# Kernel optimization log

Hardware: AMD Instinct MI355X
Metric: run time of the kernel (lower is better)

## Reference

```python
import jax, jax.numpy as jnp
import numpy as np

B, V, S = 128, 64, 40
D, H, VOC = 256, 256, 20000


def setup_inputs() -> dict:
    key = jax.random.key(0)
    ks = jax.random.split(key, 26)
    g = lambda k, shp: (jax.random.normal(k, shp, dtype=jnp.float32) * 0.02)
    inp = {}
    inp['input_seqs'] = jax.random.randint(ks[0], (B, V, S), 0, VOC + 1)
    inp['mask'] = jnp.zeros((B, V), jnp.float32)
    inp['length'] = jax.random.randint(ks[1], (B,), 1, V + 1)
    inp['seq_time_step'] = jax.random.uniform(ks[2], (B, V), dtype=jnp.float32)
    inp['codemask'] = jnp.zeros((B, V, S), jnp.float32)
    inp['label'] = jax.random.randint(ks[3], (B,), 0, 2)
    # embedding table; padding_idx=-1 in torch == row VOC zeroed
    inp['emb'] = g(ks[4], (VOC + 1, D)).at[VOC].set(0.0)
    # LSTM (single layer, batch_first): torch gate order i,f,g,o
    inp['W_ih'] = g(ks[5], (4 * H, D))
    inp['W_hh'] = g(ks[6], (4 * H, H))
    inp['b_ih'] = g(ks[7], (4 * H,))
    inp['b_hh'] = g(ks[8], (4 * H,))
    # attention projections
    inp['Whk'] = g(ks[9], (D, H))
    inp['bhk'] = g(ks[10], (D,))
    inp['W1'] = g(ks[11], (64, 2 * H))
    inp['b1'] = g(ks[12], (64,))
    inp['W2'] = g(ks[13], (2, 64))
    inp['b2'] = g(ks[14], (2,))
    # classifyer MLP: d -> 4d -> 2d -> 2
    inp['C1W'] = g(ks[15], (4 * D, D))
    inp['C1b'] = g(ks[16], (4 * D,))
    inp['C2W'] = g(ks[17], (2 * D, 4 * D))
    inp['C2b'] = g(ks[18], (2 * D,))
    inp['CoW'] = g(ks[19], (2, 2 * D))
    inp['Cob'] = g(ks[20], (2,))
    return inp


def _lstm(x, W_ih, W_hh, b_ih, b_hh):
    # x: [B,T,D] -> hs: [B,T,H]; torch gate order i,f,g,o
    Bsz = x.shape[0]
    Hd = W_hh.shape[1]
    xg = jnp.einsum('btd,gd->btg', x, W_ih) + b_ih + b_hh  # [B,T,4H]

    def step(carry, xg_t):
        h, c = carry
        gates = xg_t + h @ W_hh.T
        i, f, gg, o = jnp.split(gates, 4, axis=-1)
        i = jax.nn.sigmoid(i); f = jax.nn.sigmoid(f)
        gg = jnp.tanh(gg); o = jax.nn.sigmoid(o)
        c = f * c + i * gg
        h = o * jnp.tanh(c)
        return (h, c), h

    z = jnp.zeros((Bsz, Hd), x.dtype)
    _, hs = jax.lax.scan(step, (z, z), jnp.swapaxes(xg, 0, 1))
    return jnp.swapaxes(hs, 0, 1)


def _classify(h, C1W, C1b, C2W, C2b, CoW, Cob):
    h = jax.nn.relu(h @ C1W.T + C1b)
    h = jax.nn.relu(h @ C2W.T + C2b)
    return h @ CoW.T + Cob


def reference(input_seqs, mask, length, seq_time_step, codemask, label,
              emb, W_ih, W_hh, b_ih, b_hh, Whk, bhk, W1, b1, W2, b2,
              C1W, C1b, C2W, C2b, CoW, Cob):
    # before(): embedding gather -> relu -> sum over codes (eval mode, no dropout)
    v = jax.nn.relu(emb[input_seqs]).sum(-2)  # [B,V,D]
    h = _lstm(v, W_ih, W_hh, b_ih, b_hh)       # [B,V,H]

    # vectorized form of the per-timestep attention loop:
    # bar_v[:,0]=v[:,0]; for i>=1: mix of e_k=v[:,0] and w_hk(h[:,i-1])
    e_k = v[:, :1, :]                                   # [B,1,D]
    wh = h @ Whk.T + bhk                                # [B,V,D]
    wh_prev = wh[:, :-1, :]                             # [B,V-1,D] (h at i-1)
    e_b = jnp.broadcast_to(e_k, wh_prev.shape)
    cat = jnp.concatenate([e_b, wh_prev], axis=-1)      # [B,V-1,2D]
    attn = jax.nn.softmax(jnp.tanh(cat @ W1.T + b1) @ W2.T + b2, axis=-1)
    bar_rest = e_b * attn[..., 0:1] + wh_prev * attn[..., 1:2]
    bar_v = jnp.concatenate([v[:, :1, :], bar_rest], axis=1)  # [B,V,D]

    # GAN stand-in (external injected module): identity
    Dec_V, Gen_V = bar_v, bar_v
    gen_h = _lstm(Gen_V, W_ih, W_hh, b_ih, b_hh)

    og = _classify(h, C1W, C1b, C2W, C2b, CoW, Cob)        # [B,V,2]
    fake = _classify(gen_h, C1W, C1b, C2W, C2b, CoW, Cob)  # [B,V,2]
    final_og = og[:, -1, :]
    final_fake = fake[:, -1, :]
    return (final_og, final_fake, Dec_V, Gen_V, seq_time_step, label)
```

## Files before the change

kernel.cpp:

```cpp
#include <hip/hip_runtime.h>

#define DEV __device__ __forceinline__

typedef float f32x4 __attribute__((ext_vector_type(4)));
typedef short s16x8 __attribute__((ext_vector_type(8)));
typedef short s16x4 __attribute__((ext_vector_type(4)));

DEV unsigned short f2bf(float f){
  unsigned int u = __float_as_uint(f);
  u += 0x7fffu + ((u>>16)&1u);
  return (unsigned short)(u>>16);
}
DEV float bf2f(unsigned short h){ return __uint_as_float(((unsigned int)h)<<16); }

#if __has_builtin(__builtin_amdgcn_rcpf)
DEV float frcp_(float x){ return __builtin_amdgcn_rcpf(x); }
#else
DEV float frcp_(float x){ return 1.f/x; }
#endif
#if __has_builtin(__builtin_amdgcn_exp2f)
DEV float fexp2_(float x){ return __builtin_amdgcn_exp2f(x); }
#else
DEV float fexp2_(float x){ return exp2f(x); }
#endif

DEV float sigm(float x){ return frcp_(1.f + fexp2_(-1.4426950408889634f*x)); }
DEV float tanh_(float x){
  x = fminf(x, 30.f);
  float e = fexp2_(2.8853900817779268f*x);
  return (e-1.f)*frcp_(e+1.f);
}

DEV unsigned char f2e4m3(float x){
  unsigned int u = __float_as_uint(x);
  unsigned int s = (u>>24)&0x80u;
  unsigned int mag = u & 0x7fffffffu;
  if (mag > 0x43E00000u) mag = 0x43E00000u;
  mag += 0x000FFFFFu + ((mag>>20)&1u);
  int e = (int)(mag>>23) - 120;
  unsigned int m = (mag>>20)&7u;
  unsigned int r = (e<=0) ? 0u : (((unsigned)e<<3)|m);
  return (unsigned char)(s|r);
}

DEV f32x4 mfma_bf16(s16x8 a, s16x8 b, f32x4 c){
  return __builtin_amdgcn_mfma_f32_16x16x32_bf16(a,b,c,0,0,0);
}
DEV f32x4 mfma_fp8(long a, long b, f32x4 c){
  return __builtin_amdgcn_mfma_f32_16x16x32_fp8_fp8(a,b,c,0,0,0);
}

DEV void lds_barrier(){
  asm volatile("s_waitcnt lgkmcnt(0)\n\ts_barrier" ::: "memory");
}

#define Bx 128
#define Vx 64
#define Sx 40
#define Dx 256
#define Hx 256

#define OFF_OG   0
#define OFF_FAKE 256
#define OFF_DECV 512
#define OFF_GENV 2097664
#define OFF_STS  4194816
#define OFF_LBL  4203008

#define PW_IH  0
#define PW_HH  262144
#define PW_HK  524288
#define PW_1   589824
#define PC_1   622592
#define PC_2   884736
#define PC_O   1409024
#define P_TOT  1410048

__global__ void k_cvtall(const float* __restrict__ W_ih, const float* __restrict__ Whh,
                         const float* __restrict__ Whk, const float* __restrict__ W1,
                         const float* __restrict__ C1W, const float* __restrict__ C2W,
                         const float* __restrict__ CoW, unsigned short* __restrict__ dst,
                         unsigned char* __restrict__ dst8){
  int i = blockIdx.x*256 + threadIdx.x;
  if (i < P_TOT){
    float v;
    if      (i < PW_HH) v = W_ih[i - PW_IH];
    else if (i < PW_HK) v = Whh [i - PW_HH];
    else if (i < PW_1 ) v = Whk [i - PW_HK];
    else if (i < PC_1 ) v = W1  [i - PW_1 ];
    else if (i < PC_2 ) v = C1W [i - PC_1 ];
    else if (i < PC_O ) v = C2W [i - PC_2 ];
    else                v = CoW [i - PC_O ];
    dst[i] = f2bf(v);
  } else if (i < P_TOT + 262144){
    dst8[i - P_TOT] = f2e4m3(16.f*Whh[i - P_TOT]);
  }
}

__global__ void k_embed(const int* __restrict__ seqs, const float* __restrict__ emb,
                        float* __restrict__ v32, unsigned short* __restrict__ v16,
                        float* __restrict__ decv, float* __restrict__ genv,
                        unsigned short* __restrict__ barv16){
  int bt = blockIdx.x;
  int d = threadIdx.x;
  const int* sp = seqs + (size_t)bt*Sx;
  float acc = 0.f;
  #pragma unroll 4
  for (int s=0;s<Sx;s++){
    int id = sp[s];
    acc += fmaxf(emb[(size_t)id*Dx + d], 0.f);
  }
  size_t o = (size_t)bt*Dx + d;
  v32[o] = acc;
  v16[o] = f2bf(acc);
  if ((bt & 63) == 0){
    decv[o] = acc; genv[o] = acc; barv16[o] = f2bf(acc);
  }
}

template<int MODE_A, int MODE_C, int RELU>
__global__ void k_gemm(const unsigned short* __restrict__ A, const unsigned short* __restrict__ Bw,
                       const float* __restrict__ bias1, const float* __restrict__ bias2,
                       unsigned short* __restrict__ C, int K, int Ntot, float scale){
  int tid = threadIdx.x, w = tid>>6, l = tid&63, lm = l&15, q = l>>4;
  int m0 = blockIdx.x*64;
  int n0 = blockIdx.y*256 + w*64;
  f32x4 acc[4][4];
  #pragma unroll
  for (int nt=0;nt<4;nt++){
    int n = n0 + nt*16 + lm;
    float bz = bias1 ? bias1[n] : 0.f;
    if (bias2) bz += bias2[n];
    #pragma unroll
    for (int mt=0;mt<4;mt++) acc[mt][nt] = (f32x4){bz,bz,bz,bz};
  }
  const s16x8* Arow[4];
  #pragma unroll
  for (int mt=0;mt<4;mt++){
    int m = m0 + mt*16 + lm;
    size_t off = (MODE_A==0) ? (size_t)m*K : ((size_t)(m&127)*Vx + (m>>7))*(size_t)K;
    Arow[mt] = (const s16x8*)(A + off);
  }
  int kkn = K/32;
  for (int kk=0; kk<kkn; kk++){
    s16x8 bfr[4];
    #pragma unroll
    for (int nt=0;nt<4;nt++){
      int n = n0 + nt*16 + lm;
      bfr[nt] = *(const s16x8*)(Bw + (size_t)n*K + kk*32 + q*8);
    }
    #pragma unroll
    for (int mt=0;mt<4;mt++){
      s16x8 afr = Arow[mt][kk*4 + q];
      #pragma unroll
      for (int nt=0;nt<4;nt++)
        acc[mt][nt] = mfma_bf16(afr, bfr[nt], acc[mt][nt]);
    }
  }
  #pragma unroll
  for (int mt=0;mt<4;mt++){
    int mbase = m0 + mt*16 + q*4;
    #pragma unroll
    for (int nt=0;nt<4;nt++){
      int n = n0 + nt*16 + lm;
      if (MODE_C==0){
        #pragma unroll
        for (int r=0;r<4;r++){
          float val = scale*acc[mt][nt][r];
          if (RELU) val = fmaxf(val, 0.f);
          C[(size_t)(mbase+r)*Ntot + n] = f2bf(val);
        }
      } else {
        int tt = mbase>>7, bb = mbase&127;
        int gg = bb>>4, b4 = bb&15;
        s16x4 sv;
        #pragma unroll
        for (int r=0;r<4;r++){
          float val = scale*acc[mt][nt][r];
          if (RELU) val = fmaxf(val, 0.f);
          sv[r] = (short)f2bf(val);
        }
        *(s16x4*)(C + (((size_t)tt*8 + gg)*1024 + n)*16 + b4) = sv;
      }
    }
  }
}

#define HPB 264
template<int STORE_ALL>
__global__ __launch_bounds__(1024) void k_scan(const unsigned char* __restrict__ W8,
        const unsigned short* __restrict__ xg, unsigned short* __restrict__ hist,
        const float* __restrict__ v32, const float* __restrict__ W1,
        const float* __restrict__ b1, float* __restrict__ u,
        const float* __restrict__ sts, const int* __restrict__ label,
        float* __restrict__ out){
  int tid = threadIdx.x;
  if (STORE_ALL && blockIdx.x >= 8){
    int bid = blockIdx.x - 8;
    if (bid < 8){
      int t2 = bid*1024 + tid;
      int b = t2>>6, n = t2&63;
      const f32x4* vr = (const f32x4*)(v32 + (size_t)b*Vx*Dx);
      const f32x4* wr = (const f32x4*)(W1 + (size_t)n*512);
      float a = b1[n];
      for (int kk=0;kk<64;kk++){
        f32x4 x = vr[kk], ww = wr[kk];
        a += x[0]*ww[0] + x[1]*ww[1] + x[2]*ww[2] + x[3]*ww[3];
      }
      u[(size_t)b*64 + n] = a;
    } else {
      for (int i=tid;i<Bx*Vx;i+=1024) out[OFF_STS + i] = sts[i];
      if (tid < Bx) out[OFF_LBL + tid] = (float)label[tid];
    }
    return;
  }
  __shared__ __align__(16) unsigned char hl[2][16*HPB];
  int g = blockIdx.x;
  int w = tid>>6, l = tid&63, lm = l&15, q = l>>4;
  int j = w*16 + lm;
  for (int i=tid;i<2*16*HPB;i+=1024) ((unsigned char*)hl)[i] = 0;
  if (w & 1) asm volatile("s_setprio 1");
  long Bf[4][8];
  #pragma unroll
  for (int qq=0;qq<4;qq++){
    int n = qq*256 + j;
    #pragma unroll
    for (int kk=0;kk<8;kk++)
      Bf[qq][kk] = *(const long*)(W8 + (size_t)n*256 + kk*32 + q*8);
  }
  float cst[4] = {0.f,0.f,0.f,0.f};
  const unsigned short* xgb = xg + (size_t)g*16384 + q*4;
  s16x4 xc[4], xn[4];
  #pragma unroll
  for (int qq=0;qq<4;qq++) xc[qq] = *(const s16x4*)(xgb + (qq*256+j)*16);
  __syncthreads();
  const float K1 = 1.4426950408889634f/256.f;
  const unsigned char* hrd = hl[0] + lm*HPB + q*8;
  #pragma unroll 1
  for (int t=0;t<Vx;t++){
    if (t < Vx-1){
      #pragma unroll
      for (int qq=0;qq<4;qq++)
        xn[qq] = *(const s16x4*)(xgb + (size_t)(t+1)*131072 + (qq*256+j)*16);
    }
    const unsigned char* hb = hrd + (t&1)*(16*HPB);
    f32x4 a0;
    #pragma unroll
    for (int r=0;r<4;r++) a0[r] = bf2f((unsigned short)xc[0][r]);
    #pragma unroll
    for (int kk=0;kk<8;kk++) a0 = mfma_fp8(*(const long*)(hb + kk*32), Bf[0][kk], a0);
    float iv[4];
    #pragma unroll
    for (int r=0;r<4;r++) iv[r] = frcp_(1.f + fexp2_(-K1*a0[r]));
    f32x4 a1;
    #pragma unroll
    for (int r=0;r<4;r++) a1[r] = bf2f((unsigned short)xc[1][r]);
    #pragma unroll
    for (int kk=0;kk<8;kk++) a1 = mfma_fp8(*(const long*)(hb + kk*32), Bf[1][kk], a1);
    float fv[4];
    #pragma unroll
    for (int r=0;r<4;r++) fv[r] = frcp_(1.f + fexp2_(-K1*a1[r]));
    f32x4 a2;
    #pragma unroll
    for (int r=0;r<4;r++) a2[r] = bf2f((unsigned short)xc[2][r]);
    #pragma unroll
    for (int kk=0;kk<8;kk++) a2 = mfma_fp8(*(const long*)(hb + kk*32), Bf[2][kk], a2);
    float cvn[4];
    #pragma unroll
    for (int r=0;r<4;r++){
      float eg = fexp2_(2.f*K1*a2[r]);
      float gv = (eg-1.f)*frcp_(eg+1.f);
      cvn[r] = fv[r]*cst[r] + iv[r]*gv;
    }
    f32x4 a3;
    #pragma unroll
    for (int r=0;r<4;r++) a3[r] = bf2f((unsigned short)xc[3][r]);
    #pragma unroll
    for (int kk=0;kk<8;kk++) a3 = mfma_fp8(*(const long*)(hb + kk*32), Bf[3][kk], a3);
    unsigned char* hn = hl[(t+1)&1] + j;
    float hv16[4];
    #pragma unroll
    for (int r=0;r<4;r++){
      float ov = frcp_(1.f + fexp2_(-K1*a3[r]));
      float cv = cvn[r];
      cst[r] = cv;
      float ec = fexp2_(2.8853900817779268f*fminf(cv,30.f));
      float hv = ov*(ec-1.f)*frcp_(ec+1.f);
      hv16[r] = 16.f*hv;
      if (STORE_ALL)
        hist[((size_t)t*Bx + g*16 + q*4 + r)*Hx + j] = f2bf(hv);
      else if (t==Vx-1)
        hist[((size_t)(g*16 + q*4 + r))*Hx + j] = f2bf(hv);
    }
#if __has_builtin(__builtin_amdgcn_cvt_pk_fp8_f32)
    int p01 = __builtin_amdgcn_cvt_pk_fp8_f32(hv16[0], hv16[1], 0, false);
    int p23 = __builtin_amdgcn_cvt_pk_fp8_f32(hv16[2], hv16[3], 0, false);
    hn[(q*4+0)*HPB] = (unsigned char)p01;
    hn[(q*4+1)*HPB] = (unsigned char)(p01>>8);
    hn[(q*4+2)*HPB] = (unsigned char)p23;
    hn[(q*4+3)*HPB] = (unsigned char)(p23>>8);
#else
    #pragma unroll
    for (int r=0;r<4;r++) hn[(q*4+r)*HPB] = f2e4m3(hv16[r]);
#endif
    #pragma unroll
    for (int qq=0;qq<4;qq++) xc[qq] = xn[qq];
    lds_barrier();
  }
}

__global__ void k_attn(const unsigned short* __restrict__ wh16,
                       const float* __restrict__ v32, const float* __restrict__ u,
                       const unsigned short* __restrict__ W116, const float* __restrict__ W2,
                       const float* __restrict__ b2,
                       float* __restrict__ decv, float* __restrict__ genv,
                       unsigned short* __restrict__ barv16){
  int tid = threadIdx.x, w = tid>>6, l = tid&63, lm = l&15, q = l>>4;
  int mt = blockIdx.x*4 + w;
  int m0 = mt*16;
  f32x4 acc[4];
  #pragma unroll
  for (int nt=0;nt<4;nt++){
    int n = nt*16 + lm;
    f32x4 a;
    #pragma unroll
    for (int r=0;r<4;r++) a[r] = u[(size_t)((m0 + q*4 + r)&127)*64 + n];
    acc[nt] = a;
  }
  const s16x8* Arow = (const s16x8*)(wh16 + (size_t)(m0+lm)*Dx);
  #pragma unroll
  for (int kk=0;kk<8;kk++){
    s16x8 af = Arow[kk*4 + q];
    #pragma unroll
    for (int nt=0;nt<4;nt++){
      int n = nt*16 + lm;
      s16x8 bf = *(const s16x8*)(W116 + (size_t)n*512 + 256 + kk*32 + q*8);
      acc[nt] = mfma_bf16(af, bf, acc[nt]);
    }
  }
  float p0a[4] = {0,0,0,0}, p1a[4] = {0,0,0,0};
  #pragma unroll
  for (int nt=0;nt<4;nt++){
    int n = nt*16 + lm;
    float w2a = W2[n], w2b = W2[64+n];
    #pragma unroll
    for (int r=0;r<4;r++){
      float z = tanh_(acc[nt][r]);
      p0a[r] += z*w2a; p1a[r] += z*w2b;
    }
  }
  #pragma unroll
  for (int s=1;s<16;s<<=1){
    #pragma unroll
    for (int r=0;r<4;r++){ p0a[r] += __shfl_xor(p0a[r], s, 16); p1a[r] += __shfl_xor(p1a[r], s, 16); }
  }
  float bb0 = b2[0], bb1 = b2[1];
  int t = m0>>7;
  int d0 = lm*16;
  #pragma unroll
  for (int r=0;r<4;r++){
    int m = m0 + q*4 + r; int b = m&127;
    float a0 = p0a[r]+bb0, a1 = p1a[r]+bb1;
    float al0 = frcp_(1.f + fexp2_(1.4426950408889634f*(a1-a0)));
    float al1 = 1.f - al0;
    const f32x4* ek = (const f32x4*)(v32 + (size_t)b*Vx*Dx + d0);
    const unsigned short* whr = wh16 + (size_t)m*Dx + d0;
    size_t ob = ((size_t)b*Vx + (t+1))*Dx + d0;
    #pragma unroll
    for (int c=0;c<4;c++){
      f32x4 e = ek[c], o;
      s16x4 o16;
      #pragma unroll
      for (int jj=0;jj<4;jj++){
        o[jj] = al0*e[jj] + al1*bf2f(whr[c*4+jj]);
        o16[jj] = (short)f2bf(o[jj]);
      }
      *(f32x4*)(decv + ob + c*4) = o;
      *(f32x4*)(genv + ob + c*4) = o;
      *(s16x4*)(barv16 + ob + c*4) = o16;
    }
  }
}

__global__ void k_out(const unsigned short* __restrict__ y2, const unsigned short* __restrict__ CoW16,
                      const float* __restrict__ Cob, float* __restrict__ out){
  int tid = blockIdx.x*256 + threadIdx.x;
  int m = tid>>1, n = tid&1;
  const s16x8* yr = (const s16x8*)(y2 + (size_t)m*512);
  const s16x8* wr = (const s16x8*)(CoW16 + (size_t)n*512);
  float a = Cob[n];
  for (int kk=0;kk<64;kk++){
    s16x8 yv = yr[kk], ww = wr[kk];
    #pragma unroll
    for (int jj=0;jj<8;jj++) a += bf2f((unsigned short)yv[jj])*bf2f((unsigned short)ww[jj]);
  }
  int base = (m < 128) ? (OFF_OG + m*2) : (OFF_FAKE + (m-128)*2);
  out[base + n] = a;
}

extern "C" void kernel_launch(void* const* d_in, const int* in_sizes, int n_in,
                              void* d_out, int out_size, void* d_ws, size_t ws_size,
                              hipStream_t stream) {
  const int*   seqs  = (const int*)d_in[0];
  const float* sts   = (const float*)d_in[3];
  const int*   label = (const int*)d_in[5];
  const float* emb   = (const float*)d_in[6];
  const float* W_ih  = (const float*)d_in[7];
  const float* W_hh  = (const float*)d_in[8];
  const float* b_ih  = (const float*)d_in[9];
  const float* b_hh  = (const float*)d_in[10];
  const float* Whk   = (const float*)d_in[11];
  const float* bhk   = (const float*)d_in[12];
  const float* W1    = (const float*)d_in[13];
  const float* b1    = (const float*)d_in[14];
  const float* W2    = (const float*)d_in[15];
  const float* b2    = (const float*)d_in[16];
  const float* C1b   = (const float*)d_in[18];
  const float* C2b   = (const float*)d_in[20];
  const float* Cob   = (const float*)d_in[22];
  float* out = (float*)d_out;

  char* ws = (char*)d_ws;
  unsigned short* v16    = (unsigned short*)(ws + 0);
  unsigned short* xg     = (unsigned short*)(ws + (4<<20));
  unsigned short* hist1  = (unsigned short*)(ws + (20<<20));
  unsigned short* wh16   = (unsigned short*)(ws + (25<<20));
  unsigned short* barv16 = (unsigned short*)(ws + (29<<20));
  float*          v32    = (float*)(ws + (33<<20));
  float*          u      = (float*)(ws + (41<<20));
  unsigned char*  whh8   = (unsigned char*)(ws + (41<<20) + (512<<10));
  unsigned short* pool   = (unsigned short*)(ws + (42<<20));
  unsigned short* y1     = (unsigned short*)(ws + (45<<20));
  unsigned short* y2     = (unsigned short*)(ws + (45<<20) + (512<<10));

  unsigned short* h2 = hist1 + (size_t)Vx*Bx*Hx;
  unsigned short* X  = hist1 + (size_t)(Vx-1)*Bx*Hx;

  float* decv = out + OFF_DECV;
  float* genv = out + OFF_GENV;

  k_cvtall<<<dim3(6532), dim3(256), 0, stream>>>(W_ih, W_hh, Whk, W1,
      (const float*)d_in[17], (const float*)d_in[19], (const float*)d_in[21], pool, whh8);
  k_embed<<<dim3(Bx*Vx), dim3(256), 0, stream>>>(seqs, emb, v32, v16, decv, genv, barv16);
  k_gemm<1,1,0><<<dim3(128,4), dim3(256), 0, stream>>>(v16, pool+PW_IH, b_ih, b_hh, xg, 256, 1024, 256.f);
  k_scan<1><<<dim3(17), dim3(1024), 0, stream>>>(whh8, xg, hist1,
      v32, W1, b1, u, sts, label, out);
  k_gemm<0,0,0><<<dim3(128,1), dim3(256), 0, stream>>>(hist1, pool+PW_HK, bhk, nullptr, wh16, 256, 256, 1.f);
  k_attn<<<dim3(126), dim3(256), 0, stream>>>(wh16, v32, u, pool+PW_1, W2, b2, decv, genv, barv16);
  k_gemm<1,1,0><<<dim3(128,4), dim3(256), 0, stream>>>(barv16, pool+PW_IH, b_ih, b_hh, xg, 256, 1024, 256.f);
  k_scan<0><<<dim3(8), dim3(1024), 0, stream>>>(whh8, xg, h2,
      nullptr, nullptr, nullptr, nullptr, nullptr, nullptr, nullptr);
  k_gemm<0,0,1><<<dim3(4,4), dim3(256), 0, stream>>>(X, pool+PC_1, C1b, nullptr, y1, 256, 1024, 1.f);
  k_gemm<0,0,1><<<dim3(4,2), dim3(256), 0, stream>>>(y1, pool+PC_2, C2b, nullptr, y2, 1024, 512, 1.f);
  k_out<<<dim3(2), dim3(256), 0, stream>>>(y2, pool+PC_O, Cob, out);
}
```

Before: 597.0 us.

## Fuse both LSTM scans, attention and input GEMM into one persistent flag-synchronized kernel

Merges the first scan, the Whk projection, the attention mix, the second input-gate GEMM and the second scan into one persistent 88-block kernel. Blocks coordinate per timestep through global atomic flags, so the second LSTM can start consuming timestep t while the first is still running. Embedding, weight conversion and misc output copies are folded into one prologue kernel, and v32 is dropped in favour of bf16 v16. It also reorders the scan step so all four gate MFMAs are interleaved. The cost is spin-wait polling and a dependence on all 88 blocks being co-resident; if they are not, the kernel can deadlock.

After: 686.4 us. +15.0%, slower.

```diff
diff --git a/kernel.cpp b/kernel.cpp
--- a/kernel.cpp
+++ b/kernel.cpp
@@ -24,7 +24,6 @@
 DEV float fexp2_(float x){ return exp2f(x); }
 #endif
 
-DEV float sigm(float x){ return frcp_(1.f + fexp2_(-1.4426950408889634f*x)); }
 DEV float tanh_(float x){
   x = fminf(x, 30.f);
   float e = fexp2_(2.8853900817779268f*x);
@@ -54,6 +53,19 @@
   asm volatile("s_waitcnt lgkmcnt(0)\n\ts_barrier" ::: "memory");
 }
 
+DEV unsigned aload_acq(unsigned* p){
+  return __hip_atomic_load(p, __ATOMIC_ACQUIRE, __HIP_MEMORY_SCOPE_AGENT);
+}
+DEV void astore_rel(unsigned* p, unsigned v){
+  __hip_atomic_store(p, v, __ATOMIC_RELEASE, __HIP_MEMORY_SCOPE_AGENT);
+}
+DEV void aadd_rel(unsigned* p, unsigned v){
+  __hip_atomic_fetch_add(p, v, __ATOMIC_RELEASE, __HIP_MEMORY_SCOPE_AGENT);
+}
+DEV void spin_ge(unsigned* p, unsigned tgt){
+  while (aload_acq(p) < tgt) __builtin_amdgcn_s_sleep(2);
+}
+
 #define Bx 128
 #define Vx 64
 #define Sx 40
@@ -76,46 +88,52 @@
 #define PC_O   1409024
 #define P_TOT  1410048
 
-__global__ void k_cvtall(const float* __restrict__ W_ih, const float* __restrict__ Whh,
-                         const float* __restrict__ Whk, const float* __restrict__ W1,
-                         const float* __restrict__ C1W, const float* __restrict__ C2W,
-                         const float* __restrict__ CoW, unsigned short* __restrict__ dst,
-                         unsigned char* __restrict__ dst8){
-  int i = blockIdx.x*256 + threadIdx.x;
-  if (i < P_TOT){
-    float v;
-    if      (i < PW_HH) v = W_ih[i - PW_IH];
-    else if (i < PW_HK) v = Whh [i - PW_HH];
-    else if (i < PW_1 ) v = Whk [i - PW_HK];
-    else if (i < PC_1 ) v = W1  [i - PW_1 ];
-    else if (i < PC_2 ) v = C1W [i - PC_1 ];
-    else if (i < PC_O ) v = C2W [i - PC_2 ];
-    else                v = CoW [i - PC_O ];
-    dst[i] = f2bf(v);
-  } else if (i < P_TOT + 262144){
-    dst8[i - P_TOT] = f2e4m3(16.f*Whh[i - P_TOT]);
-  }
-}
-
-__global__ void k_embed(const int* __restrict__ seqs, const float* __restrict__ emb,
-                        float* __restrict__ v32, unsigned short* __restrict__ v16,
-                        float* __restrict__ decv, float* __restrict__ genv,
-                        unsigned short* __restrict__ barv16){
-  int bt = blockIdx.x;
-  int d = threadIdx.x;
-  const int* sp = seqs + (size_t)bt*Sx;
-  float acc = 0.f;
-  #pragma unroll 4
-  for (int s=0;s<Sx;s++){
-    int id = sp[s];
-    acc += fmaxf(emb[(size_t)id*Dx + d], 0.f);
-  }
-  size_t o = (size_t)bt*Dx + d;
-  v32[o] = acc;
-  v16[o] = f2bf(acc);
-  if ((bt & 63) == 0){
-    decv[o] = acc; genv[o] = acc; barv16[o] = f2bf(acc);
-  }
+#define HPB 264
+#define WHP 272
+
+__global__ void k_pre(const int* __restrict__ seqs, const float* __restrict__ emb,
+                      unsigned short* __restrict__ v16,
+                      float* __restrict__ decv, float* __restrict__ genv,
+                      unsigned short* __restrict__ barv16,
+                      const float* __restrict__ W_ih, const float* __restrict__ Whh,
+                      const float* __restrict__ Whk, const float* __restrict__ W1,
+                      const float* __restrict__ C1W, const float* __restrict__ C2W,
+                      const float* __restrict__ CoW,
+                      unsigned short* __restrict__ pool, unsigned char* __restrict__ whh8,
+                      const float* __restrict__ sts, const int* __restrict__ label,
+                      float* __restrict__ out, unsigned* __restrict__ flags){
+  int bx = blockIdx.x, tid = threadIdx.x;
+  if (bx < 8192){
+    int bt = bx, d = tid;
+    const int* sp = seqs + (size_t)bt*Sx;
+    float acc = 0.f;
+    #pragma unroll 4
+    for (int s=0;s<Sx;s++) acc += fmaxf(emb[(size_t)sp[s]*Dx + d], 0.f);
+    size_t o = (size_t)bt*Dx + d;
+    v16[o] = f2bf(acc);
+    if ((bt & 63) == 0){ decv[o] = acc; genv[o] = acc; barv16[o] = f2bf(acc); }
+    return;
+  }
+  if (bx < 14724){
+    int i = (bx-8192)*256 + tid;
+    if (i < P_TOT){
+      float v;
+      if      (i < PW_HH) v = W_ih[i - PW_IH];
+      else if (i < PW_HK) v = Whh [i - PW_HH];
+      else if (i < PW_1 ) v = Whk [i - PW_HK];
+      else if (i < PC_1 ) v = W1  [i - PW_1 ];
+      else if (i < PC_2 ) v = C1W [i - PC_1 ];
+      else if (i < PC_O ) v = C2W [i - PC_2 ];
+      else                v = CoW [i - PC_O ];
+      pool[i] = f2bf(v);
+    } else if (i < P_TOT + 262144){
+      whh8[i - P_TOT] = f2e4m3(16.f*Whh[i - P_TOT]);
+    }
+    return;
+  }
+  if (tid < 200) flags[tid] = (tid==64) ? 1u : 0u;
+  for (int i=tid;i<Bx*Vx;i+=256) out[OFF_STS + i] = sts[i];
+  if (tid < Bx) out[OFF_LBL + tid] = (float)label[tid];
 }
 
 template<int MODE_A, int MODE_C, int RELU>
@@ -172,54 +190,24 @@
         }
       } else {
         int tt = mbase>>7, bb = mbase&127;
-        int gg = bb>>4, b4 = bb&15;
+        int gg = bb>>4;
         s16x4 sv;
         #pragma unroll
-        for (int r=0;r<4;r++){
-          float val = scale*acc[mt][nt][r];
-          if (RELU) val = fmaxf(val, 0.f);
-          sv[r] = (short)f2bf(val);
-        }
-        *(s16x4*)(C + (((size_t)tt*8 + gg)*1024 + n)*16 + b4) = sv;
-      }
-    }
-  }
-}
-
-#define HPB 264
-template<int STORE_ALL>
-__global__ __launch_bounds__(1024) void k_scan(const unsigned char* __restrict__ W8,
-        const unsigned short* __restrict__ xg, unsigned short* __restrict__ hist,
-        const float* __restrict__ v32, const float* __restrict__ W1,
-        const float* __restrict__ b1, float* __restrict__ u,
-        const float* __restrict__ sts, const int* __restrict__ label,
-        float* __restrict__ out){
+        for (int r=0;r<4;r++) sv[r] = (short)f2bf(scale*acc[mt][nt][r]);
+        *(s16x4*)(C + (((size_t)tt*8 + gg)*1024 + n)*16 + (bb&15)) = sv;
+      }
+    }
+  }
+}
+
+template<int IS1>
+DEV void scan_body(unsigned char* hl, const unsigned char* __restrict__ W8,
+                   const unsigned short* __restrict__ xg, unsigned short* __restrict__ hist,
+                   int g, unsigned* __restrict__ ctr1, unsigned* __restrict__ xgf){
   int tid = threadIdx.x;
-  if (STORE_ALL && blockIdx.x >= 8){
-    int bid = blockIdx.x - 8;
-    if (bid < 8){
-      int t2 = bid*1024 + tid;
-      int b = t2>>6, n = t2&63;
-      const f32x4* vr = (const f32x4*)(v32 + (size_t)b*Vx*Dx);
-      const f32x4* wr = (const f32x4*)(W1 + (size_t)n*512);
-      float a = b1[n];
-      for (int kk=0;kk<64;kk++){
-        f32x4 x = vr[kk], ww = wr[kk];
-        a += x[0]*ww[0] + x[1]*ww[1] + x[2]*ww[2] + x[3]*ww[3];
-      }
-      u[(size_t)b*64 + n] = a;
-    } else {
-      for (int i=tid;i<Bx*Vx;i+=1024) out[OFF_STS + i] = sts[i];
-      if (tid < Bx) out[OFF_LBL + tid] = (float)label[tid];
-    }
-    return;
-  }
-  __shared__ __align__(16) unsigned char hl[2][16*HPB];
-  int g = blockIdx.x;
   int w = tid>>6, l = tid&63, lm = l&15, q = l>>4;
   int j = w*16 + lm;
-  for (int i=tid;i<2*16*HPB;i+=1024) ((unsigned char*)hl)[i] = 0;
-  if (w & 1) asm volatile("s_setprio 1");
+  for (int i=tid;i<2*16*HPB;i+=1024) hl[i] = 0;
   long Bf[4][8];
   #pragma unroll
   for (int qq=0;qq<4;qq++){
@@ -231,63 +219,52 @@
   float cst[4] = {0.f,0.f,0.f,0.f};
   const unsigned short* xgb = xg + (size_t)g*16384 + q*4;
   s16x4 xc[4], xn[4];
+  if (!IS1) spin_ge(&xgf[0], 1);
   #pragma unroll
   for (int qq=0;qq<4;qq++) xc[qq] = *(const s16x4*)(xgb + (qq*256+j)*16);
   __syncthreads();
   const float K1 = 1.4426950408889634f/256.f;
-  const unsigned char* hrd = hl[0] + lm*HPB + q*8;
+  const unsigned char* hrd = hl + lm*HPB + q*8;
   #pragma unroll 1
   for (int t=0;t<Vx;t++){
     if (t < Vx-1){
+      if (!IS1) spin_ge(&xgf[t+1], 1);
       #pragma unroll
       for (int qq=0;qq<4;qq++)
         xn[qq] = *(const s16x4*)(xgb + (size_t)(t+1)*131072 + (qq*256+j)*16);
     }
     const unsigned char* hb = hrd + (t&1)*(16*HPB);
-    f32x4 a0;
-    #pragma unroll
-    for (int r=0;r<4;r++) a0[r] = bf2f((unsigned short)xc[0][r]);
-    #pragma unroll
-    for (int kk=0;kk<8;kk++) a0 = mfma_fp8(*(const long*)(hb + kk*32), Bf[0][kk], a0);
-    float iv[4];
-    #pragma unroll
-    for (int r=0;r<4;r++) iv[r] = frcp_(1.f + fexp2_(-K1*a0[r]));
-    f32x4 a1;
-    #pragma unroll
-    for (int r=0;r<4;r++) a1[r] = bf2f((unsigned short)xc[1][r]);
-    #pragma unroll
-    for (int kk=0;kk<8;kk++) a1 = mfma_fp8(*(const long*)(hb + kk*32), Bf[1][kk], a1);
-    float fv[4];
-    #pragma unroll
-    for (int r=0;r<4;r++) fv[r] = frcp_(1.f + fexp2_(-K1*a1[r]));
-    f32x4 a2;
-    #pragma unroll
-    for (int r=0;r<4;r++) a2[r] = bf2f((unsigned short)xc[2][r]);
-    #pragma unroll
-    for (int kk=0;kk<8;kk++) a2 = mfma_fp8(*(const long*)(hb + kk*32), Bf[2][kk], a2);
-    float cvn[4];
+    f32x4 a0, a1, a2, a3;
     #pragma unroll
     for (int r=0;r<4;r++){
+      a0[r] = bf2f((unsigned short)xc[0][r]);
+      a1[r] = bf2f((unsigned short)xc[1][r]);
+      a2[r] = bf2f((unsigned short)xc[2][r]);
+      a3[r] = bf2f((unsigned short)xc[3][r]);
+    }
+    #pragma unroll
+    for (int kk=0;kk<8;kk++){
+      long af = *(const long*)(hb + kk*32);
+      a0 = mfma_fp8(af, Bf[0][kk], a0);
+      a1 = mfma_fp8(af, Bf[1][kk], a1);
+      a2 = mfma_fp8(af, Bf[2][kk], a2);
+      a3 = mfma_fp8(af, Bf[3][kk], a3);
+    }
+    unsigned char* hn = hl + ((t+1)&1)*(16*HPB) + j;
+    float hv16[4];
+    #pragma unroll
+    for (int r=0;r<4;r++){
+      float iv = frcp_(1.f + fexp2_(-K1*a0[r]));
+      float fv = frcp_(1.f + fexp2_(-K1*a1[r]));
       float eg = fexp2_(2.f*K1*a2[r]);
       float gv = (eg-1.f)*frcp_(eg+1.f);
-      cvn[r] = fv[r]*cst[r] + iv[r]*gv;
-    }
-    f32x4 a3;
-    #pragma unroll
-    for (int r=0;r<4;r++) a3[r] = bf2f((unsigned short)xc[3][r]);
-    #pragma unroll
-    for (int kk=0;kk<8;kk++) a3 = mfma_fp8(*(const long*)(hb + kk*32), Bf[3][kk], a3);
-    unsigned char* hn = hl[(t+1)&1] + j;
-    float hv16[4];
-    #pragma unroll
-    for (int r=0;r<4;r++){
       float ov = frcp_(1.f + fexp2_(-K1*a3[r]));
-      float cv = cvn[r];
+      float cv = fv*cst[r] + iv*gv;
       cst[r] = cv;
       float ec = fexp2_(2.8853900817779268f*fminf(cv,30.f));
       float hv = ov*(ec-1.f)*frcp_(ec+1.f);
       hv16[r] = 16.f*hv;
-      if (STORE_ALL)
+      if (IS1)
         hist[((size_t)t*Bx + g*16 + q*4 + r)*Hx + j] = f2bf(hv);
       else if (t==Vx-1)
         hist[((size_t)(g*16 + q*4 + r))*Hx + j] = f2bf(hv);
@@ -305,80 +282,204 @@
 #endif
     #pragma unroll
     for (int qq=0;qq<4;qq++) xc[qq] = xn[qq];
-    lds_barrier();
-  }
-}
-
-__global__ void k_attn(const unsigned short* __restrict__ wh16,
-                       const float* __restrict__ v32, const float* __restrict__ u,
-                       const unsigned short* __restrict__ W116, const float* __restrict__ W2,
-                       const float* __restrict__ b2,
-                       float* __restrict__ decv, float* __restrict__ genv,
-                       unsigned short* __restrict__ barv16){
+    if (IS1){
+      __syncthreads();
+      if (tid == 0) aadd_rel(&ctr1[t], 1);
+    } else {
+      lds_barrier();
+    }
+  }
+}
+
+DEV void worker_body(unsigned short* whs, int t,
+    const unsigned short* __restrict__ hist1, const unsigned short* __restrict__ v16,
+    const float* __restrict__ u, const unsigned short* __restrict__ pool,
+    const float* __restrict__ bhk, const float* __restrict__ W2, const float* __restrict__ b2,
+    const float* __restrict__ b_ih, const float* __restrict__ b_hh,
+    float* __restrict__ decv, float* __restrict__ genv,
+    unsigned short* __restrict__ barv16, unsigned short* __restrict__ xg2,
+    unsigned* ctr1, unsigned* bvf, unsigned* xgf, unsigned* uctr){
   int tid = threadIdx.x, w = tid>>6, l = tid&63, lm = l&15, q = l>>4;
-  int mt = blockIdx.x*4 + w;
-  int m0 = mt*16;
-  f32x4 acc[4];
+  if (t < 63){
+    spin_ge(&ctr1[t], 8);
+    int r0 = (w&7)*16, n0 = (w>>3)*128;
+    const s16x8* Arow = (const s16x8*)(hist1 + ((size_t)t*Bx + r0 + lm)*Hx);
+    f32x4 acc[8];
+    #pragma unroll
+    for (int nt=0;nt<8;nt++){
+      float bz = bhk[n0 + nt*16 + lm];
+      acc[nt] = (f32x4){bz,bz,bz,bz};
+    }
+    #pragma unroll
+    for (int kk=0;kk<8;kk++){
+      s16x8 afr = Arow[kk*4 + q];
+      #pragma unroll
+      for (int nt=0;nt<8;nt++){
+        int n = n0 + nt*16 + lm;
+        s16x8 bfr = *(const s16x8*)(pool + PW_HK + (size_t)n*256 + kk*32 + q*8);
+        acc[nt] = mfma_bf16(afr, bfr, acc[nt]);
+      }
+    }
+    #pragma unroll
+    for (int nt=0;nt<8;nt++){
+      int n = n0 + nt*16 + lm, mb = r0 + q*4;
+      #pragma unroll
+      for (int r=0;r<4;r++) whs[(size_t)(mb+r)*WHP + n] = f2bf(acc[nt][r]);
+    }
+    spin_ge(uctr, 8);
+    __syncthreads();
+    if (w < 8){
+      int m0l = w*16;
+      f32x4 a2[4];
+      #pragma unroll
+      for (int nt=0;nt<4;nt++){
+        int n = nt*16 + lm;
+        #pragma unroll
+        for (int r=0;r<4;r++) a2[nt][r] = u[(size_t)(m0l + q*4 + r)*64 + n];
+      }
+      #pragma unroll
+      for (int kk=0;kk<8;kk++){
+        s16x8 afr = *(const s16x8*)(whs + (size_t)(m0l+lm)*WHP + kk*32 + q*8);
+        #pragma unroll
+        for (int nt=0;nt<4;nt++){
+          int n = nt*16 + lm;
+          s16x8 bfr = *(const s16x8*)(pool + PW_1 + (size_t)n*512 + 256 + kk*32 + q*8);
+          a2[nt] = mfma_bf16(afr, bfr, a2[nt]);
+        }
+      }
+      float p0a[4] = {0,0,0,0}, p1a[4] = {0,0,0,0};
+      #pragma unroll
+      for (int nt=0;nt<4;nt++){
+        int n = nt*16 + lm;
+        float w2a = W2[n], w2b = W2[64+n];
+        #pragma unroll
+        for (int r=0;r<4;r++){
+          float z = tanh_(a2[nt][r]);
+          p0a[r] += z*w2a; p1a[r] += z*w2b;
+        }
+      }
+      #pragma unroll
+      for (int s=1;s<16;s<<=1){
+        #pragma unroll
+        for (int r=0;r<4;r++){ p0a[r] += __shfl_xor(p0a[r], s, 16); p1a[r] += __shfl_xor(p1a[r], s, 16); }
+      }
+      float bb0 = b2[0], bb1 = b2[1];
+      int d0 = lm*16;
+      #pragma unroll
+      for (int r=0;r<4;r++){
+        int b = m0l + q*4 + r;
+        float g0 = p0a[r]+bb0, g1 = p1a[r]+bb1;
+        float al0 = frcp_(1.f + fexp2_(1.4426950408889634f*(g1-g0)));
+        float al1 = 1.f - al0;
+        const unsigned short* ek  = v16 + (size_t)b*Vx*Dx + d0;
+        const unsigned short* whp = whs + (size_t)b*WHP + d0;
+        size_t ob = ((size_t)b*Vx + (t+1))*Dx + d0;
+        #pragma unroll
+        for (int c=0;c<2;c++){
+          s16x8 e8 = *(const s16x8*)(ek + c*8);
+          s16x8 w8 = *(const s16x8*)(whp + c*8);
+          s16x8 o16;
+          #pragma unroll
+          for (int jj=0;jj<8;jj++){
+            float o = al0*bf2f((unsigned short)e8[jj]) + al1*bf2f((unsigned short)w8[jj]);
+            decv[ob + c*8 + jj] = o;
+            genv[ob + c*8 + jj] = o;
+            o16[jj] = (short)f2bf(o);
+          }
+          *(s16x8*)(barv16 + ob + c*8) = o16;
+        }
+      }
+    }
+    __syncthreads();
+    if (tid == 0) astore_rel(&bvf[t+1], 1);
+  }
+  spin_ge(&bvf[t], 1);
+  int mh = (w&1)*64, nb = (w>>1)*128;
+  const s16x8* Arow2[4];
   #pragma unroll
-  for (int nt=0;nt<4;nt++){
-    int n = nt*16 + lm;
-    f32x4 a;
-    #pragma unroll
-    for (int r=0;r<4;r++) a[r] = u[(size_t)((m0 + q*4 + r)&127)*64 + n];
-    acc[nt] = a;
-  }
-  const s16x8* Arow = (const s16x8*)(wh16 + (size_t)(m0+lm)*Dx);
-  #pragma unroll
-  for (int kk=0;kk<8;kk++){
-    s16x8 af = Arow[kk*4 + q];
-    #pragma unroll
-    for (int nt=0;nt<4;nt++){
-      int n = nt*16 + lm;
-      s16x8 bf = *(const s16x8*)(W116 + (size_t)n*512 + 256 + kk*32 + q*8);
-      acc[nt] = mfma_bf16(af, bf, acc[nt]);
-    }
-  }
-  float p0a[4] = {0,0,0,0}, p1a[4] = {0,0,0,0};
-  #pragma unroll
-  for (int nt=0;nt<4;nt++){
-    int n = nt*16 + lm;
-    float w2a = W2[n], w2b = W2[64+n];
-    #pragma unroll
-    for (int r=0;r<4;r++){
-      float z = tanh_(acc[nt][r]);
-      p0a[r] += z*w2a; p1a[r] += z*w2b;
-    }
-  }
-  #pragma unroll
-  for (int s=1;s<16;s<<=1){
-    #pragma unroll
-    for (int r=0;r<4;r++){ p0a[r] += __shfl_xor(p0a[r], s, 16); p1a[r] += __shfl_xor(p1a[r], s, 16); }
-  }
-  float bb0 = b2[0], bb1 = b2[1];
-  int t = m0>>7;
-  int d0 = lm*16;
-  #pragma unroll
-  for (int r=0;r<4;r++){
-    int m = m0 + q*4 + r; int b = m&127;
-    float a0 = p0a[r]+bb0, a1 = p1a[r]+bb1;
-    float al0 = frcp_(1.f + fexp2_(1.4426950408889634f*(a1-a0)));
-    float al1 = 1.f - al0;
-    const f32x4* ek = (const f32x4*)(v32 + (size_t)b*Vx*Dx + d0);
-    const unsigned short* whr = wh16 + (size_t)m*Dx + d0;
-    size_t ob = ((size_t)b*Vx + (t+1))*Dx + d0;
-    #pragma unroll
-    for (int c=0;c<4;c++){
-      f32x4 e = ek[c], o;
-      s16x4 o16;
-      #pragma unroll
-      for (int jj=0;jj<4;jj++){
-        o[jj] = al0*e[jj] + al1*bf2f(whr[c*4+jj]);
-        o16[jj] = (short)f2bf(o[jj]);
-      }
-      *(f32x4*)(decv + ob + c*4) = o;
-      *(f32x4*)(genv + ob + c*4) = o;
-      *(s16x4*)(barv16 + ob + c*4) = o16;
-    }
+  for (int mt=0;mt<4;mt++)
+    Arow2[mt] = (const s16x8*)(barv16 + ((size_t)(mh + mt*16 + lm)*Vx + t)*Dx);
+  #pragma unroll 1
+  for (int sc=0; sc<4; sc++){
+    int n0 = nb + sc*32;
+    f32x4 acc[4][2];
+    #pragma unroll
+    for (int nt=0;nt<2;nt++){
+      int n = n0 + nt*16 + lm;
+      float bz = b_ih[n] + b_hh[n];
+      #pragma unroll
+      for (int mt=0;mt<4;mt++) acc[mt][nt] = (f32x4){bz,bz,bz,bz};
+    }
+    #pragma unroll
+    for (int kk=0;kk<8;kk++){
+      s16x8 bfr[2];
+      #pragma unroll
+      for (int nt=0;nt<2;nt++){
+        int n = n0 + nt*16 + lm;
+        bfr[nt] = *(const s16x8*)(pool + PW_IH + (size_t)n*256 + kk*32 + q*8);
+      }
+      #pragma unroll
+      for (int mt=0;mt<4;mt++){
+        s16x8 afr = Arow2[mt][kk*4 + q];
+        acc[mt][0] = mfma_bf16(afr, bfr[0], acc[mt][0]);
+        acc[mt][1] = mfma_bf16(afr, bfr[1], acc[mt][1]);
+      }
+    }
+    #pragma unroll
+    for (int mt=0;mt<4;mt++){
+      int m = mh + mt*16 + q*4;
+      int gg = m>>4;
+      #pragma unroll
+      for (int nt=0;nt<2;nt++){
+        int n = n0 + nt*16 + lm;
+        s16x4 sv;
+        #pragma unroll
+        for (int r=0;r<4;r++) sv[r] = (short)f2bf(256.f*acc[mt][nt][r]);
+        *(s16x4*)(xg2 + (((size_t)t*8 + gg)*1024 + n)*16 + (m&15)) = sv;
+      }
+    }
+  }
+  __syncthreads();
+  if (tid == 0) astore_rel(&xgf[t], 1);
+}
+
+__global__ __launch_bounds__(1024) void k_mega(
+    const unsigned char* __restrict__ W8,
+    const unsigned short* __restrict__ xg1, unsigned short* __restrict__ xg2,
+    unsigned short* __restrict__ hist1, unsigned short* __restrict__ h2,
+    const unsigned short* __restrict__ v16, float* __restrict__ u,
+    const unsigned short* __restrict__ pool,
+    const float* __restrict__ bhk, const float* __restrict__ W2, const float* __restrict__ b2,
+    const float* __restrict__ b1, const float* __restrict__ b_ih, const float* __restrict__ b_hh,
+    float* __restrict__ decv, float* __restrict__ genv, unsigned short* __restrict__ barv16,
+    unsigned* __restrict__ flags){
+  __shared__ __align__(16) unsigned char smem[69632];
+  unsigned* ctr1 = flags;
+  unsigned* bvf  = flags + 64;
+  unsigned* xgf  = flags + 128;
+  unsigned* uctr = flags + 192;
+  int blk = blockIdx.x;
+  if (blk < 8){
+    scan_body<1>(smem, W8, xg1, hist1, blk, ctr1, xgf);
+  } else if (blk < 16){
+    scan_body<0>(smem, W8, xg2, h2, blk-8, ctr1, xgf);
+  } else if (blk < 80){
+    worker_body((unsigned short*)smem, blk-16, hist1, v16, u, pool, bhk, W2, b2,
+                b_ih, b_hh, decv, genv, barv16, xg2, ctr1, bvf, xgf, uctr);
+  } else {
+    int t2 = (blk-80)*1024 + threadIdx.x;
+    int b = t2>>6, n = t2&63;
+    const s16x8* vr = (const s16x8*)(v16 + (size_t)b*Vx*Dx);
+    const s16x8* wr = (const s16x8*)(pool + PW_1 + (size_t)n*512);
+    float a = b1[n];
+    for (int kk=0;kk<32;kk++){
+      s16x8 x = vr[kk], ww = wr[kk];
+      #pragma unroll
+      for (int jj=0;jj<8;jj++) a += bf2f((unsigned short)x[jj])*bf2f((unsigned short)ww[jj]);
+    }
+    u[t2] = a;
+    __syncthreads();
+    if (threadIdx.x == 0) aadd_rel(uctr, 1);
   }
 }
 
@@ -422,16 +523,16 @@
 
   char* ws = (char*)d_ws;
   unsigned short* v16    = (unsigned short*)(ws + 0);
-  unsigned short* xg     = (unsigned short*)(ws + (4<<20));
+  unsigned short* xg1    = (unsigned short*)(ws + (4<<20));
   unsigned short* hist1  = (unsigned short*)(ws + (20<<20));
-  unsigned short* wh16   = (unsigned short*)(ws + (25<<20));
-  unsigned short* barv16 = (unsigned short*)(ws + (29<<20));
-  float*          v32    = (float*)(ws + (33<<20));
-  float*          u      = (float*)(ws + (41<<20));
-  unsigned char*  whh8   = (unsigned char*)(ws + (41<<20) + (512<<10));
-  unsigned short* pool   = (unsigned short*)(ws + (42<<20));
-  unsigned short* y1     = (unsigned short*)(ws + (45<<20));
-  unsigned short* y2     = (unsigned short*)(ws + (45<<20) + (512<<10));
+  unsigned short* barv16 = (unsigned short*)(ws + (25<<20));
+  unsigned short* xg2    = (unsigned short*)(ws + (29<<20));
+  float*          u      = (float*)(ws + (45<<20));
+  unsigned char*  whh8   = (unsigned char*)(ws + (45<<20) + (64<<10));
+  unsigned*       flags  = (unsigned*)(ws + (45<<20) + (320<<10));
+  unsigned short* pool   = (unsigned short*)(ws + (45<<20) + (512<<10));
+  unsigned short* y1     = xg1;
+  unsigned short* y2     = xg1 + 262144;
 
   unsigned short* h2 = hist1 + (size_t)Vx*Bx*Hx;
   unsigned short* X  = hist1 + (size_t)(Vx-1)*Bx*Hx;
@@ -439,17 +540,12 @@
   float* decv = out + OFF_DECV;
   float* genv = out + OFF_GENV;
 
-  k_cvtall<<<dim3(6532), dim3(256), 0, stream>>>(W_ih, W_hh, Whk, W1,
-      (const float*)d_in[17], (const float*)d_in[19], (const float*)d_in[21], pool, whh8);
-  k_embed<<<dim3(Bx*Vx), dim3(256), 0, stream>>>(seqs, emb, v32, v16, decv, genv, barv16);
-  k_gemm<1,1,0><<<dim3(128,4), dim3(256), 0, stream>>>(v16, pool+PW_IH, b_ih, b_hh, xg, 256, 1024, 256.f);
-  k_scan<1><<<dim3(17), dim3(1024), 0, stream>>>(whh8, xg, hist1,
-      v32, W1, b1, u, sts, label, out);
-  k_gemm<0,0,0><<<dim3(128,1), dim3(256), 0, stream>>>(hist1, pool+PW_HK, bhk, nullptr, wh16, 256, 256, 1.f);
-  k_attn<<<dim3(126), dim3(256), 0, stream>>>(wh16, v32, u, pool+PW_1, W2, b2, decv, genv, barv16);
-  k_gemm<1,1,0><<<dim3(128,4), dim3(256), 0, stream>>>(barv16, pool+PW_IH, b_ih, b_hh, xg, 256, 1024, 256.f);
-  k_scan<0><<<dim3(8), dim3(1024), 0, stream>>>(whh8, xg, h2,
-      nullptr, nullptr, nullptr, nullptr, nullptr, nullptr, nullptr);
+  k_pre<<<dim3(14725), dim3(256), 0, stream>>>(seqs, emb, v16, decv, genv, barv16,
+      W_ih, W_hh, Whk, W1, (const float*)d_in[17], (const float*)d_in[19],
+      (const float*)d_in[21], pool, whh8, sts, label, out, flags);
+  k_gemm<1,1,0><<<dim3(128,4), dim3(256), 0, stream>>>(v16, pool+PW_IH, b_ih, b_hh, xg1, 256, 1024, 256.f);
+  k_mega<<<dim3(88), dim3(1024), 0, stream>>>(whh8, xg1, xg2, hist1, h2, v16, u, pool,
+      bhk, W2, b2, b1, b_ih, b_hh, decv, genv, barv16, flags);
   k_gemm<0,0,1><<<dim3(4,4), dim3(256), 0, stream>>>(X, pool+PC_1, C1b, nullptr, y1, 256, 1024, 1.f);
   k_gemm<0,0,1><<<dim3(4,2), dim3(256), 0, stream>>>(y1, pool+PC_2, C2b, nullptr, y2, 1024, 512, 1.f);
   k_out<<<dim3(2), dim3(256), 0, stream>>>(y2, pool+PC_O, Cob, out);
```
